# Optimization experiments

Hardware: AMD Instinct MI355X
Metric: run time of the kernel (lower is better)

The kernel has to match this reference:

```python
import jax, jax.numpy as jnp
import numpy as np

D_MODEL = 2048
ADAPTER = 64


def setup_inputs() -> dict:
    key = jax.random.key(0)
    k_x, k_dw, k_uw = jax.random.split(key, 3)
    x = jax.random.normal(k_x, (4, 4096, D_MODEL), dtype=jnp.float32)
    # LayerNorm params (torch defaults: weight=1, bias=0)
    ln_w = jnp.ones((D_MODEL,), dtype=jnp.float32)
    ln_b = jnp.zeros((D_MODEL,), dtype=jnp.float32)
    # down: Linear(d_model -> adapter), weight std=0.01, bias=0
    down_w = 0.01 * jax.random.normal(k_dw, (ADAPTER, D_MODEL), dtype=jnp.float32)
    down_b = jnp.zeros((ADAPTER,), dtype=jnp.float32)
    # up: Linear(adapter -> d_model), weight std=init_scale=1e-3, bias=0
    up_w = 1e-3 * jax.random.normal(k_uw, (D_MODEL, ADAPTER), dtype=jnp.float32)
    up_b = jnp.zeros((D_MODEL,), dtype=jnp.float32)
    return {"x": x, "ln_w": ln_w, "ln_b": ln_b,
            "down_w": down_w, "down_b": down_b,
            "up_w": up_w, "up_b": up_b}


def layer_norm(x, w, b, eps=1e-5):
    mu = jnp.mean(x, axis=-1, keepdims=True)
    var = jnp.mean(jnp.square(x - mu), axis=-1, keepdims=True)
    return (x - mu) * jax.lax.rsqrt(var + eps) * w + b


def reference(x, ln_w, ln_b, down_w, down_b, up_w, up_b):
    # x: (B, T, D)
    h = layer_norm(x, ln_w, ln_b)
    h = jax.nn.relu(jnp.einsum('btd,ad->bta', h, down_w) + down_b)  # (B,T,A)
    h = jnp.einsum('bta,da->btd', h, up_w) + up_b                   # (B,T,D)
    return x + h
```

## Files before the change

### kernel.cpp

```cpp
#include <hip/hip_runtime.h>

#define D_MODEL 2048
#define ADAPTER 64
#define RPB     16
#define THREADS 256
#define NROWS   16384

typedef __attribute__((ext_vector_type(4))) float f32x4;
typedef __attribute__((ext_vector_type(8))) short bf16x8;
typedef __attribute__((ext_vector_type(4))) unsigned short u16x4;
typedef __attribute__((ext_vector_type(8))) unsigned short u16x8;

__device__ __forceinline__ unsigned short f2bf(float f) {
    unsigned int u = __float_as_uint(f);
    u += 0x7fffu + ((u >> 16) & 1u);
    return (unsigned short)(u >> 16);
}
__device__ __forceinline__ float bf2f(unsigned short u) {
    return __uint_as_float(((unsigned int)u) << 16);
}

__global__ __launch_bounds__(256)
void weights_to_bf16(const float* __restrict__ dw, const float* __restrict__ uw,
                     unsigned short* __restrict__ dwb, unsigned short* __restrict__ uwb)
{
    const int i = 4 * (blockIdx.x * 256 + threadIdx.x);
    f32x4 a = *(const f32x4*)(dw + i);
    f32x4 b = *(const f32x4*)(uw + i);
    u16x4 ra, rb;
#pragma unroll
    for (int j = 0; j < 4; ++j) { ra[j] = f2bf(a[j]); rb[j] = f2bf(b[j]); }
    *(u16x4*)(dwb + i) = ra;
    *(u16x4*)(uwb + i) = rb;
}

__global__ __launch_bounds__(THREADS, 2)
void houlsby_fused(const float* __restrict__ x,
                   const float* __restrict__ lnw,
                   const float* __restrict__ lnb,
                   const unsigned short* __restrict__ dwb,
                   const float* __restrict__ db,
                   const unsigned short* __restrict__ uwb,
                   const float* __restrict__ ub,
                   float* __restrict__ out)
{
    __shared__ __align__(16) unsigned short xl[RPB * D_MODEL];
    __shared__ __align__(16) unsigned short lwl[D_MODEL];
    __shared__ __align__(16) unsigned short lbl[D_MODEL];
    __shared__ float stats_mu[RPB];
    __shared__ float stats_rs[RPB];
    __shared__ __align__(16) unsigned short Hl[RPB][ADAPTER + 8];

    const int tid = threadIdx.x;
    const int w   = tid >> 6;
    const int l   = tid & 63;
    const int rowBase = blockIdx.x * RPB;

#pragma unroll
    for (int j = 0; j < 2; ++j) {
        const int c4 = tid + 256 * j;
        f32x4 a = *(const f32x4*)(lnw + 4 * c4);
        f32x4 b = *(const f32x4*)(lnb + 4 * c4);
        u16x4 ra, rb;
#pragma unroll
        for (int k = 0; k < 4; ++k) { ra[k] = f2bf(a[k]); rb[k] = f2bf(b[k]); }
        *(u16x4*)(lwl + 4 * c4) = ra;
        *(u16x4*)(lbl + 4 * c4) = rb;
    }

    for (int rr = 0; rr < 4; ++rr) {
        const int row = 4 * w + rr;
        const float* xr = x + (size_t)(rowBase + row) * D_MODEL;
        char* xrow_l = (char*)(xl + row * D_MODEL);
        const int swz = (row & 7) << 4;
        float s = 0.f, sq = 0.f;
#pragma unroll
        for (int j = 0; j < 8; ++j) {
            f32x4 v = *(const f32x4*)(xr + 4 * l + 256 * j);
            s  += v.x + v.y + v.z + v.w;
            sq += v.x * v.x + v.y * v.y + v.z * v.z + v.w * v.w;
            u16x4 hv;
#pragma unroll
            for (int k = 0; k < 4; ++k) hv[k] = f2bf(v[k]);
            const int boff = ((4 * l + 256 * j) * 2) ^ swz;
            *(u16x4*)(xrow_l + boff) = hv;
        }
#pragma unroll
        for (int off = 32; off; off >>= 1) {
            s  += __shfl_xor(s,  off, 64);
            sq += __shfl_xor(sq, off, 64);
        }
        if (l == 0) {
            const float mu  = s * (1.f / D_MODEL);
            const float var = sq * (1.f / D_MODEL) - mu * mu;
            stats_mu[row] = mu;
            stats_rs[row] = rsqrtf(var + 1e-5f);
        }
    }
    __syncthreads();

    const int m  = l & 15;
    const int g  = l >> 4;

    const float mu  = stats_mu[m];
    const float rs  = stats_rs[m];
    const float nmr = -mu * rs;

    const int a0 = 16 * w + m;
    const unsigned short* dwr = dwb + a0 * D_MODEL;
    const char* xrow_l = (const char*)(xl + m * D_MODEL);
    const int swzm = (m & 7) << 4;

    f32x4 acc = {0.f, 0.f, 0.f, 0.f};

#pragma unroll 4
    for (int ks = 0; ks < 64; ++ks) {
        const int kb = 32 * ks + 8 * g;
        u16x8 xv = *(const u16x8*)(xrow_l + ((2 * kb) ^ swzm));
        u16x8 lwv = *(const u16x8*)(lwl + kb);
        u16x8 lbv = *(const u16x8*)(lbl + kb);
        bf16x8 af;
#pragma unroll
        for (int jj = 0; jj < 8; ++jj) {
            const float xf = bf2f(xv[jj]);
            const float v  = fmaf(fmaf(xf, rs, nmr), bf2f(lwv[jj]), bf2f(lbv[jj]));
            af[jj] = (short)f2bf(v);
        }
        const bf16x8 bw = *(const bf16x8*)(dwr + kb);
        acc = __builtin_amdgcn_mfma_f32_16x16x32_bf16(af, bw, acc, 0, 0, 0);
    }

    {
        const float dbv = db[a0];
#pragma unroll
        for (int r = 0; r < 4; ++r) {
            const float h = fmaxf(acc[r] + dbv, 0.f);
            Hl[4 * g + r][a0] = f2bf(h);
        }
    }
    __syncthreads();

    bf16x8 Hf[2];
#pragma unroll
    for (int ks = 0; ks < 2; ++ks)
        Hf[ks] = *(const bf16x8*)(&Hl[m][32 * ks + 8 * g]);

    const int dBase = 512 * w;
    const size_t orow = (size_t)(rowBase + m) * D_MODEL;
#pragma unroll 2
    for (int nt = 0; nt < 32; ++nt) {
        const int d0 = dBase + 16 * nt;
        const unsigned short* uwr = uwb + (d0 + m) * ADAPTER;
        const bf16x8 A0 = *(const bf16x8*)(uwr + 8 * g);
        const bf16x8 A1 = *(const bf16x8*)(uwr + 32 + 8 * g);

        f32x4 c = {0.f, 0.f, 0.f, 0.f};
        c = __builtin_amdgcn_mfma_f32_16x16x32_bf16(A0, Hf[0], c, 0, 0, 0);
        c = __builtin_amdgcn_mfma_f32_16x16x32_bf16(A1, Hf[1], c, 0, 0, 0);

        const int dcol = d0 + 4 * g;
        const f32x4 ubv = *(const f32x4*)(ub + dcol);
        const u16x4 xres = *(const u16x4*)(xrow_l + ((2 * dcol) ^ swzm));
        f32x4 o;
#pragma unroll
        for (int r = 0; r < 4; ++r)
            o[r] = bf2f(xres[r]) + c[r] + ubv[r];
        *(f32x4*)(out + orow + dcol) = o;
    }
}

extern "C" void kernel_launch(void* const* d_in, const int* in_sizes, int n_in,
                              void* d_out, int out_size, void* d_ws, size_t ws_size,
                              hipStream_t stream) {
    const float* x   = (const float*)d_in[0];
    const float* lnw = (const float*)d_in[1];
    const float* lnb = (const float*)d_in[2];
    const float* dw  = (const float*)d_in[3];
    const float* db  = (const float*)d_in[4];
    const float* uw  = (const float*)d_in[5];
    const float* ub  = (const float*)d_in[6];
    float* out = (float*)d_out;

    unsigned short* dwb = (unsigned short*)d_ws;
    unsigned short* uwb = (unsigned short*)((char*)d_ws + 64 * 2048 * 2);

    weights_to_bf16<<<dim3(128), dim3(256), 0, stream>>>(dw, uw, dwb, uwb);

    dim3 grid(NROWS / RPB);
    dim3 block(THREADS);
    houlsby_fused<<<grid, block, 0, stream>>>(x, lnw, lnb, dwb, db, uwb, ub, out);
}
```

Baseline: 289.1 us.

## Normalize rows once in LDS and read residual from fp32 input

LayerNorm is now applied once per row in a pass over shared memory. Previously each wave redid the normalize-and-convert work for every k-step inside the down-projection MFMA loop. The GEMM loop now only loads bf16 operands and issues MFMAs, which removes redundant ALU work and the shared-memory staging of LN weights and stats. The residual add now re-reads fp32 x from global memory instead of using the bf16 copy, which fixes precision but adds a second pass of input traffic. Unroll factors on both loops are also raised.

Measured after the change: 303.5 us. 1.05x slower.

```diff
diff --git a/kernel.cpp b/kernel.cpp
--- a/kernel.cpp
+++ b/kernel.cpp
@@ -45,10 +45,6 @@
                    float* __restrict__ out)
 {
     __shared__ __align__(16) unsigned short xl[RPB * D_MODEL];
-    __shared__ __align__(16) unsigned short lwl[D_MODEL];
-    __shared__ __align__(16) unsigned short lbl[D_MODEL];
-    __shared__ float stats_mu[RPB];
-    __shared__ float stats_rs[RPB];
     __shared__ __align__(16) unsigned short Hl[RPB][ADAPTER + 8];
 
     const int tid = threadIdx.x;
@@ -56,18 +52,7 @@
     const int l   = tid & 63;
     const int rowBase = blockIdx.x * RPB;
 
-#pragma unroll
-    for (int j = 0; j < 2; ++j) {
-        const int c4 = tid + 256 * j;
-        f32x4 a = *(const f32x4*)(lnw + 4 * c4);
-        f32x4 b = *(const f32x4*)(lnb + 4 * c4);
-        u16x4 ra, rb;
-#pragma unroll
-        for (int k = 0; k < 4; ++k) { ra[k] = f2bf(a[k]); rb[k] = f2bf(b[k]); }
-        *(u16x4*)(lwl + 4 * c4) = ra;
-        *(u16x4*)(lbl + 4 * c4) = rb;
-    }
-
+    float rsv[4], nmrv[4];
     for (int rr = 0; rr < 4; ++rr) {
         const int row = 4 * w + rr;
         const float* xr = x + (size_t)(rowBase + row) * D_MODEL;
@@ -82,29 +67,47 @@
             u16x4 hv;
 #pragma unroll
             for (int k = 0; k < 4; ++k) hv[k] = f2bf(v[k]);
-            const int boff = ((4 * l + 256 * j) * 2) ^ swz;
-            *(u16x4*)(xrow_l + boff) = hv;
+            *(u16x4*)(xrow_l + (((4 * l + 256 * j) * 2) ^ swz)) = hv;
         }
 #pragma unroll
         for (int off = 32; off; off >>= 1) {
             s  += __shfl_xor(s,  off, 64);
             sq += __shfl_xor(sq, off, 64);
         }
-        if (l == 0) {
-            const float mu  = s * (1.f / D_MODEL);
-            const float var = sq * (1.f / D_MODEL) - mu * mu;
-            stats_mu[row] = mu;
-            stats_rs[row] = rsqrtf(var + 1e-5f);
+        const float mu  = s * (1.f / D_MODEL);
+        const float var = sq * (1.f / D_MODEL) - mu * mu;
+        const float rs  = rsqrtf(var + 1e-5f);
+        rsv[rr]  = rs;
+        nmrv[rr] = -mu * rs;
+    }
+
+    for (int rr = 0; rr < 4; ++rr) {
+        const int row = 4 * w + rr;
+        char* xrow_l = (char*)(xl + row * D_MODEL);
+        const int swz = (row & 7) << 4;
+        const float rs = rsv[rr], nmr = nmrv[rr];
+#pragma unroll
+        for (int j = 0; j < 4; ++j) {
+            const int e0 = 8 * l + 512 * j;
+            char* p = xrow_l + ((2 * e0) ^ swz);
+            u16x8 xv = *(const u16x8*)p;
+            f32x4 lw0 = *(const f32x4*)(lnw + e0);
+            f32x4 lw1 = *(const f32x4*)(lnw + e0 + 4);
+            f32x4 lb0 = *(const f32x4*)(lnb + e0);
+            f32x4 lb1 = *(const f32x4*)(lnb + e0 + 4);
+            u16x8 hv;
+#pragma unroll
+            for (int k = 0; k < 4; ++k) {
+                hv[k]     = f2bf(fmaf(fmaf(bf2f(xv[k]),     rs, nmr), lw0[k], lb0[k]));
+                hv[4 + k] = f2bf(fmaf(fmaf(bf2f(xv[4 + k]), rs, nmr), lw1[k], lb1[k]));
+            }
+            *(u16x8*)p = hv;
         }
     }
     __syncthreads();
 
     const int m  = l & 15;
     const int g  = l >> 4;
-
-    const float mu  = stats_mu[m];
-    const float rs  = stats_rs[m];
-    const float nmr = -mu * rs;
 
     const int a0 = 16 * w + m;
     const unsigned short* dwr = dwb + a0 * D_MODEL;
@@ -113,19 +116,10 @@
 
     f32x4 acc = {0.f, 0.f, 0.f, 0.f};
 
-#pragma unroll 4
+#pragma unroll 8
     for (int ks = 0; ks < 64; ++ks) {
         const int kb = 32 * ks + 8 * g;
-        u16x8 xv = *(const u16x8*)(xrow_l + ((2 * kb) ^ swzm));
-        u16x8 lwv = *(const u16x8*)(lwl + kb);
-        u16x8 lbv = *(const u16x8*)(lbl + kb);
-        bf16x8 af;
-#pragma unroll
-        for (int jj = 0; jj < 8; ++jj) {
-            const float xf = bf2f(xv[jj]);
-            const float v  = fmaf(fmaf(xf, rs, nmr), bf2f(lwv[jj]), bf2f(lbv[jj]));
-            af[jj] = (short)f2bf(v);
-        }
+        const bf16x8 af = *(const bf16x8*)(xrow_l + ((2 * kb) ^ swzm));
         const bf16x8 bw = *(const bf16x8*)(dwr + kb);
         acc = __builtin_amdgcn_mfma_f32_16x16x32_bf16(af, bw, acc, 0, 0, 0);
     }
@@ -147,7 +141,7 @@
 
     const int dBase = 512 * w;
     const size_t orow = (size_t)(rowBase + m) * D_MODEL;
-#pragma unroll 2
+#pragma unroll 4
     for (int nt = 0; nt < 32; ++nt) {
         const int d0 = dBase + 16 * nt;
         const unsigned short* uwr = uwb + (d0 + m) * ADAPTER;
@@ -159,12 +153,12 @@
         c = __builtin_amdgcn_mfma_f32_16x16x32_bf16(A1, Hf[1], c, 0, 0, 0);
 
         const int dcol = d0 + 4 * g;
-        const f32x4 ubv = *(const f32x4*)(ub + dcol);
-        const u16x4 xres = *(const u16x4*)(xrow_l + ((2 * dcol) ^ swzm));
+        const f32x4 ubv  = *(const f32x4*)(ub + dcol);
+        const f32x4 xres = *(const f32x4*)(x + orow + dcol);
         f32x4 o;
 #pragma unroll
         for (int r = 0; r < 4; ++r)
-            o[r] = bf2f(xres[r]) + c[r] + ubv[r];
+            o[r] = xres[r] + c[r] + ubv[r];
         *(f32x4*)(out + orow + dcol) = o;
     }
 }
```

## Fold LayerNorm affine into down-projection weights and halve rows per block

Applied to the files above, without the earlier changes.

Precomputes gamma-scaled down weights in bf16, plus per-adapter row sums T and bias constants C, so the kernel feeds raw bf16 x straight into MFMA and applies mean/rstd afterwards as h = rs*(acc - mu*T) + C. This removes the per-element normalize/convert work from the down-projection inner loop and the per-block LN parameter conversion. Rows per block drop from 16 to 8 with a higher occupancy hint, which duplicates rows inside each 16-row MFMA tile and masks half the stores. The trade-off is wasted MFMA work and extra cancellation error from subtracting mu*T after accumulating unnormalized x in bf16.

Result: slower. 340.4 us (+17.8%).

```diff
diff --git a/kernel.cpp b/kernel.cpp
--- a/kernel.cpp
+++ b/kernel.cpp
@@ -2,7 +2,7 @@
 
 #define D_MODEL 2048
 #define ADAPTER 64
-#define RPB     16
+#define RPB     8
 #define THREADS 256
 #define NROWS   16384
 
@@ -21,35 +21,70 @@
 }
 
 __global__ __launch_bounds__(256)
-void weights_to_bf16(const float* __restrict__ dw, const float* __restrict__ uw,
-                     unsigned short* __restrict__ dwb, unsigned short* __restrict__ uwb)
+void prep_weights(const float* __restrict__ dw, const float* __restrict__ lnw,
+                  const float* __restrict__ lnb, const float* __restrict__ db,
+                  const float* __restrict__ uw,
+                  unsigned short* __restrict__ dwl, float* __restrict__ T,
+                  float* __restrict__ CC, unsigned short* __restrict__ uwb)
 {
-    const int i = 4 * (blockIdx.x * 256 + threadIdx.x);
-    f32x4 a = *(const f32x4*)(dw + i);
-    f32x4 b = *(const f32x4*)(uw + i);
-    u16x4 ra, rb;
-#pragma unroll
-    for (int j = 0; j < 4; ++j) { ra[j] = f2bf(a[j]); rb[j] = f2bf(b[j]); }
-    *(u16x4*)(dwb + i) = ra;
-    *(u16x4*)(uwb + i) = rb;
-}
-
-__global__ __launch_bounds__(THREADS, 2)
+    __shared__ float redT[4], redC[4];
+    const int b = blockIdx.x;
+    const int tid = threadIdx.x;
+    if (b < 64) {
+        const int a = b;
+        const float* dr = dw + a * D_MODEL;
+        float tpart = 0.f, cpart = 0.f;
+#pragma unroll
+        for (int j = 0; j < 2; ++j) {
+            const int e = 4 * tid + 1024 * j;
+            f32x4 wv = *(const f32x4*)(dr + e);
+            f32x4 gv = *(const f32x4*)(lnw + e);
+            f32x4 bv = *(const f32x4*)(lnb + e);
+            u16x4 o;
+#pragma unroll
+            for (int k = 0; k < 4; ++k) {
+                const unsigned short h = f2bf(wv[k] * gv[k]);
+                o[k] = h;
+                tpart += bf2f(h);
+                cpart += wv[k] * bv[k];
+            }
+            *(u16x4*)(dwl + a * D_MODEL + e) = o;
+        }
+#pragma unroll
+        for (int off = 32; off; off >>= 1) {
+            tpart += __shfl_xor(tpart, off, 64);
+            cpart += __shfl_xor(cpart, off, 64);
+        }
+        const int w = tid >> 6, l = tid & 63;
+        if (l == 0) { redT[w] = tpart; redC[w] = cpart; }
+        __syncthreads();
+        if (tid == 0) {
+            T[a]  = redT[0] + redT[1] + redT[2] + redT[3];
+            CC[a] = redC[0] + redC[1] + redC[2] + redC[3] + db[a];
+        }
+    } else {
+        const int i = 4 * ((b - 64) * 256 + tid);
+        f32x4 v = *(const f32x4*)(uw + i);
+        u16x4 r;
+#pragma unroll
+        for (int k = 0; k < 4; ++k) r[k] = f2bf(v[k]);
+        *(u16x4*)(uwb + i) = r;
+    }
+}
+
+__global__ __launch_bounds__(THREADS, 4)
 void houlsby_fused(const float* __restrict__ x,
-                   const float* __restrict__ lnw,
-                   const float* __restrict__ lnb,
-                   const unsigned short* __restrict__ dwb,
-                   const float* __restrict__ db,
+                   const unsigned short* __restrict__ dwl,
+                   const float* __restrict__ T,
+                   const float* __restrict__ CC,
                    const unsigned short* __restrict__ uwb,
                    const float* __restrict__ ub,
                    float* __restrict__ out)
 {
     __shared__ __align__(16) unsigned short xl[RPB * D_MODEL];
-    __shared__ __align__(16) unsigned short lwl[D_MODEL];
-    __shared__ __align__(16) unsigned short lbl[D_MODEL];
+    __shared__ __align__(16) unsigned short Hl[16][ADAPTER + 8];
     __shared__ float stats_mu[RPB];
     __shared__ float stats_rs[RPB];
-    __shared__ __align__(16) unsigned short Hl[RPB][ADAPTER + 8];
 
     const int tid = threadIdx.x;
     const int w   = tid >> 6;
@@ -57,22 +92,11 @@
     const int rowBase = blockIdx.x * RPB;
 
 #pragma unroll
-    for (int j = 0; j < 2; ++j) {
-        const int c4 = tid + 256 * j;
-        f32x4 a = *(const f32x4*)(lnw + 4 * c4);
-        f32x4 b = *(const f32x4*)(lnb + 4 * c4);
-        u16x4 ra, rb;
-#pragma unroll
-        for (int k = 0; k < 4; ++k) { ra[k] = f2bf(a[k]); rb[k] = f2bf(b[k]); }
-        *(u16x4*)(lwl + 4 * c4) = ra;
-        *(u16x4*)(lbl + 4 * c4) = rb;
-    }
-
-    for (int rr = 0; rr < 4; ++rr) {
-        const int row = 4 * w + rr;
+    for (int rr = 0; rr < 2; ++rr) {
+        const int row = 2 * w + rr;
         const float* xr = x + (size_t)(rowBase + row) * D_MODEL;
         char* xrow_l = (char*)(xl + row * D_MODEL);
-        const int swz = (row & 7) << 4;
+        const int swz = row << 4;
         float s = 0.f, sq = 0.f;
 #pragma unroll
         for (int j = 0; j < 8; ++j) {
@@ -82,8 +106,7 @@
             u16x4 hv;
 #pragma unroll
             for (int k = 0; k < 4; ++k) hv[k] = f2bf(v[k]);
-            const int boff = ((4 * l + 256 * j) * 2) ^ swz;
-            *(u16x4*)(xrow_l + boff) = hv;
+            *(u16x4*)(xrow_l + (((4 * l + 256 * j) * 2) ^ swz)) = hv;
         }
 #pragma unroll
         for (int off = 32; off; off >>= 1) {
@@ -101,40 +124,29 @@
 
     const int m  = l & 15;
     const int g  = l >> 4;
-
-    const float mu  = stats_mu[m];
-    const float rs  = stats_rs[m];
-    const float nmr = -mu * rs;
-
     const int a0 = 16 * w + m;
-    const unsigned short* dwr = dwb + a0 * D_MODEL;
-    const char* xrow_l = (const char*)(xl + m * D_MODEL);
-    const int swzm = (m & 7) << 4;
+    const int mrow = m & 7;
+    const unsigned short* dwr = dwl + a0 * D_MODEL;
+    const char* xrow_l = (const char*)(xl + mrow * D_MODEL);
+    const int swzm = mrow << 4;
 
     f32x4 acc = {0.f, 0.f, 0.f, 0.f};
-
-#pragma unroll 4
+#pragma unroll 8
     for (int ks = 0; ks < 64; ++ks) {
         const int kb = 32 * ks + 8 * g;
-        u16x8 xv = *(const u16x8*)(xrow_l + ((2 * kb) ^ swzm));
-        u16x8 lwv = *(const u16x8*)(lwl + kb);
-        u16x8 lbv = *(const u16x8*)(lbl + kb);
-        bf16x8 af;
-#pragma unroll
-        for (int jj = 0; jj < 8; ++jj) {
-            const float xf = bf2f(xv[jj]);
-            const float v  = fmaf(fmaf(xf, rs, nmr), bf2f(lwv[jj]), bf2f(lbv[jj]));
-            af[jj] = (short)f2bf(v);
-        }
+        const bf16x8 af = *(const bf16x8*)(xrow_l + ((2 * kb) ^ swzm));
         const bf16x8 bw = *(const bf16x8*)(dwr + kb);
         acc = __builtin_amdgcn_mfma_f32_16x16x32_bf16(af, bw, acc, 0, 0, 0);
     }
 
     {
-        const float dbv = db[a0];
+        const float Ta = T[a0];
+        const float Ca = CC[a0];
 #pragma unroll
         for (int r = 0; r < 4; ++r) {
-            const float h = fmaxf(acc[r] + dbv, 0.f);
+            const int t = (4 * g + r) & 7;
+            const float pre = fmaf(-stats_mu[t], Ta, acc[r]);
+            const float h   = fmaxf(fmaf(stats_rs[t], pre, Ca), 0.f);
             Hl[4 * g + r][a0] = f2bf(h);
         }
     }
@@ -146,8 +158,8 @@
         Hf[ks] = *(const bf16x8*)(&Hl[m][32 * ks + 8 * g]);
 
     const int dBase = 512 * w;
-    const size_t orow = (size_t)(rowBase + m) * D_MODEL;
-#pragma unroll 2
+    const size_t orow = (size_t)(rowBase + mrow) * D_MODEL;
+#pragma unroll 4
     for (int nt = 0; nt < 32; ++nt) {
         const int d0 = dBase + 16 * nt;
         const unsigned short* uwr = uwb + (d0 + m) * ADAPTER;
@@ -158,14 +170,16 @@
         c = __builtin_amdgcn_mfma_f32_16x16x32_bf16(A0, Hf[0], c, 0, 0, 0);
         c = __builtin_amdgcn_mfma_f32_16x16x32_bf16(A1, Hf[1], c, 0, 0, 0);
 
-        const int dcol = d0 + 4 * g;
-        const f32x4 ubv = *(const f32x4*)(ub + dcol);
-        const u16x4 xres = *(const u16x4*)(xrow_l + ((2 * dcol) ^ swzm));
-        f32x4 o;
-#pragma unroll
-        for (int r = 0; r < 4; ++r)
-            o[r] = bf2f(xres[r]) + c[r] + ubv[r];
-        *(f32x4*)(out + orow + dcol) = o;
+        if (m < 8) {
+            const int dcol = d0 + 4 * g;
+            const f32x4 ubv  = *(const f32x4*)(ub + dcol);
+            const u16x4 xres = *(const u16x4*)(xrow_l + ((2 * dcol) ^ swzm));
+            f32x4 o;
+#pragma unroll
+            for (int r = 0; r < 4; ++r)
+                o[r] = bf2f(xres[r]) + c[r] + ubv[r];
+            *(f32x4*)(out + orow + dcol) = o;
+        }
     }
 }
 
@@ -181,12 +195,15 @@
     const float* ub  = (const float*)d_in[6];
     float* out = (float*)d_out;
 
-    unsigned short* dwb = (unsigned short*)d_ws;
-    unsigned short* uwb = (unsigned short*)((char*)d_ws + 64 * 2048 * 2);
-
-    weights_to_bf16<<<dim3(128), dim3(256), 0, stream>>>(dw, uw, dwb, uwb);
+    unsigned short* dwl = (unsigned short*)d_ws;
+    float*          Tp  = (float*)((char*)d_ws + 262144);
+    float*          CCp = (float*)((char*)d_ws + 262144 + 256);
+    unsigned short* uwb = (unsigned short*)((char*)d_ws + 262144 + 512);
+
+    prep_weights<<<dim3(192), dim3(256), 0, stream>>>(dw, lnw, lnb, db, uw,
+                                                      dwl, Tp, CCp, uwb);
 
     dim3 grid(NROWS / RPB);
     dim3 block(THREADS);
-    houlsby_fused<<<grid, block, 0, stream>>>(x, lnw, lnb, dwb, db, uwb, ub, out);
-}
+    houlsby_fused<<<grid, block, 0, stream>>>(x, dwl, Tp, CCp, uwb, ub, out);
+}
```
